# Performance work log

Hardware: AMD Instinct MI355X
Metric: run time of the kernel (lower is better)

The kernel has to match this reference:

```python
import jax, jax.numpy as jnp
import numpy as np

N_NODES = 100000
N_GRAPHS = 64

def gcn_conv(x, edge_index, W, b, num_nodes):
    # PyG GCNConv: x' = D^-1/2 (A + I) D^-1/2 (x W) + b
    h = x @ W  # [N, out]
    row, col = edge_index[0], edge_index[1]
    loops = jnp.arange(num_nodes, dtype=row.dtype)
    src = jnp.concatenate([row, loops])  # message source (x_j)
    dst = jnp.concatenate([col, loops])  # aggregation target
    deg = jax.ops.segment_sum(jnp.ones_like(src, dtype=h.dtype), dst,
                              num_segments=num_nodes)
    dinv = jnp.where(deg > 0, jax.lax.rsqrt(deg), 0.0)
    norm = dinv[src] * dinv[dst]  # [E+N]
    msgs = h[src] * norm[:, None]  # gather-transform
    out = jax.ops.segment_sum(msgs, dst, num_segments=num_nodes)  # scatter
    return out + b

def global_mean_pool(x, batch, num_graphs):
    sums = jax.ops.segment_sum(x, batch, num_segments=num_graphs)
    cnts = jax.ops.segment_sum(jnp.ones((x.shape[0],), x.dtype), batch,
                               num_segments=num_graphs)
    return sums / jnp.maximum(cnts, 1.0)[:, None]

def setup_inputs() -> dict:
    key = jax.random.key(0)
    ks = jax.random.split(key, 12)
    d_in, d_hid, d_mid, d_out = 128, 128, 20, 10
    n_edges = 1600000
    x = jax.random.normal(ks[0], (N_NODES, d_in), dtype=jnp.float32)
    edge_index = jax.random.randint(ks[1], (2, n_edges), 0, N_NODES, dtype=jnp.int64)
    batch = jnp.sort(jax.random.randint(ks[2], (N_NODES,), 0, N_GRAPHS, dtype=jnp.int64))
    def glorot(k, fan_in, fan_out):
        s = (6.0 / (fan_in + fan_out)) ** 0.5
        return jax.random.uniform(k, (fan_in, fan_out), jnp.float32, -s, s)
    return {
        "x": x, "edge_index": edge_index, "batch": batch,
        "W1": glorot(ks[3], d_in, d_hid), "b1": jnp.zeros((d_hid,), jnp.float32),
        "W2": glorot(ks[4], d_hid, d_hid), "b2": jnp.zeros((d_hid,), jnp.float32),
        "fc1_W": glorot(ks[5], d_hid, d_mid), "fc1_b": jnp.zeros((d_mid,), jnp.float32),
        "fc2_W": glorot(ks[6], d_mid, d_out), "fc2_b": jnp.zeros((d_out,), jnp.float32),
    }

def reference(x, edge_index, batch, W1, b1, W2, b2, fc1_W, fc1_b, fc2_W, fc2_b):
    # eval mode: dropout is identity
    h = gcn_conv(x, edge_index, W1, b1, N_NODES)
    h = jax.nn.elu(h)
    h = gcn_conv(h, edge_index, W2, b2, N_NODES)
    g = global_mean_pool(h, batch, N_GRAPHS)  # [G, hidden]
    g = jax.nn.relu(g @ fc1_W + fc1_b)
    g = g @ fc2_W + fc2_b
    return jax.nn.log_softmax(g, axis=1)
```

## Files before the change

### kernel.cpp

```cpp
#include <hip/hip_runtime.h>
#include <math.h>

#define DH 128
#define BCAP 16384

typedef __bf16 bf8_t __attribute__((ext_vector_type(8)));
typedef short short8 __attribute__((ext_vector_type(8)));
typedef float f4_t __attribute__((ext_vector_type(4)));
typedef float f2_t __attribute__((ext_vector_type(2)));

__device__ inline unsigned short f2b(float f) {
    unsigned int u = __builtin_bit_cast(unsigned int, f);
    u = u + 0x7fffu + ((u >> 16) & 1u);
    return (unsigned short)(u >> 16);
}
__device__ inline float b2f(unsigned short h) {
    return __builtin_bit_cast(float, (unsigned int)h << 16);
}

__global__ __launch_bounds__(256) void k_bucket(const int* __restrict__ row,
                                                const int* __restrict__ col,
                                                int E, int nbuck, int chunk,
                                                unsigned int* __restrict__ pairs,
                                                int* __restrict__ bcur) {
    __shared__ int lcnt[256];
    __shared__ int lbase[256];
    __shared__ unsigned int srec[2048];
    int t = threadIdx.x;
    int e0 = blockIdx.x * chunk;
    int e1 = min(e0 + chunk, E);
    lcnt[t] = 0;
    __syncthreads();
    for (int i = e0 + t; i < e1; i += 256) {
        int d = col[i];
        int b = d >> 9;
        int slot = atomicAdd(&lcnt[b], 1);
        srec[i - e0] = ((unsigned int)b << 22) | ((unsigned int)(d & 511) << 13)
                     | (unsigned int)slot;
    }
    __syncthreads();
    if (t < nbuck) {
        int c = lcnt[t];
        lbase[t] = (c > 0) ? atomicAdd(&bcur[t * 16], c) : 0;
    }
    __syncthreads();
    for (int i = e0 + t; i < e1; i += 256) {
        unsigned int r = srec[i - e0];
        int b = r >> 22;
        unsigned int dl = (r >> 13) & 511u;
        int slot = (int)(r & 8191u);
        int g = lbase[b] + slot;
        if (g < BCAP)
            pairs[(size_t)b * BCAP + g] = ((unsigned int)row[i] << 9) | dl;
    }
}

__global__ __launch_bounds__(512) void k_build(const unsigned int* __restrict__ pairs,
                                               const int* __restrict__ bcur,
                                               int nbuck, int N,
                                               int* __restrict__ off,
                                               int* __restrict__ dpd,
                                               float* __restrict__ dinv,
                                               int* __restrict__ csr) {
    __shared__ int cnt2[512];
    __shared__ int scn[512];
    __shared__ int curi[512];
    int b = blockIdx.x, t = threadIdx.x;
    int cnt = min(bcur[b * 16], BCAP);
    int base = b * BCAP;
    int node0 = b << 9;
    int nodes = min(512, N - node0);
    cnt2[t] = (t < nodes) ? 1 : 0;
    __syncthreads();
    const unsigned int* pp = pairs + (size_t)b * BCAP;
    for (int i = t; i < cnt; i += 512)
        atomicAdd(&cnt2[pp[i] & 511u], 1);
    __syncthreads();
    int c = cnt2[t];
    int pdv = (c + 15) & ~15;
    scn[t] = pdv;
    __syncthreads();
    for (int d = 1; d < 512; d <<= 1) {
        int v = (t >= d) ? scn[t - d] : 0;
        __syncthreads();
        scn[t] += v;
        __syncthreads();
    }
    int exc = min(scn[t] - pdv, BCAP);
    int avail = BCAP - exc;
    int pdc = min(pdv, avail);
    curi[t] = exc + 1;
    if (t < nodes) {
        off[node0 + t] = base + exc;
        dpd[node0 + t] = pdc;
        dinv[node0 + t] = rsqrtf((float)c);
        if (pdc > 0) csr[base + exc] = node0 + t;
        for (int k = c; k < pdc; k++) csr[base + exc + k] = N;
    }
    __syncthreads();
    for (int i = t; i < cnt; i += 512) {
        unsigned int p = pp[i];
        int d = (int)(p & 511u);
        int slot = atomicAdd(&curi[d], 1);
        if (slot < BCAP) csr[base + slot] = (int)(p >> 9);
    }
}

__global__ void k_prepW(const float* __restrict__ W1, const float* __restrict__ W2,
                        unsigned short* __restrict__ Wt1, unsigned short* __restrict__ Wt2,
                        unsigned int* __restrict__ t8zrow) {
    int t = blockIdx.x * blockDim.x + threadIdx.x;
    if (blockIdx.x == 0 && threadIdx.x < 32) t8zrow[threadIdx.x] = 0u;
    int v = t & 16383;
    int k = v >> 7, n = v & 127;
    if (t < 16384) {
        Wt1[n * DH + k] = f2b(W1[k * DH + n]);
    } else {
        int p = ((k & 15) << 3) | (k >> 4);
        Wt2[n * DH + p] = f2b(W2[k * DH + n]);
    }
}

__global__ __launch_bounds__(256) void k_gemm_mfma(const void* __restrict__ Xin, int x_is_bf16,
                                                   const unsigned short* __restrict__ Wt,
                                                   const float* __restrict__ dinv,
                                                   unsigned char* __restrict__ Y, int nrows) {
    __shared__ unsigned short Xs[64 * 136];
    __shared__ unsigned short Ws[128 * 136];
    int t = threadIdx.x;
    int row0 = blockIdx.x * 64;

    for (int v = t; v < 128 * 32; v += 256) {
        int n = v >> 5, kq = v & 31;
        ushort4 w = ((const ushort4*)Wt)[v];
        *(ushort4*)&Ws[n * 136 + kq * 4] = w;
    }
    if (x_is_bf16) {
        const unsigned short* X = (const unsigned short*)Xin;
        for (int v = t; v < 64 * 32; v += 256) {
            int r = v >> 5, cq = v & 31;
            int gr = row0 + r;
            ushort4 h;
            if (gr < nrows) h = ((const ushort4*)X)[(size_t)gr * 32 + cq];
            else { h.x = 0; h.y = 0; h.z = 0; h.w = 0; }
            *(ushort4*)&Xs[r * 136 + cq * 4] = h;
        }
    } else {
        const float* X = (const float*)Xin;
        for (int v = t; v < 64 * 32; v += 256) {
            int r = v >> 5, cq = v & 31;
            int gr = row0 + r;
            ushort4 h;
            if (gr < nrows) {
                float4 xv = ((const float4*)X)[(size_t)gr * 32 + cq];
                h.x = f2b(xv.x); h.y = f2b(xv.y); h.z = f2b(xv.z); h.w = f2b(xv.w);
            } else { h.x = 0; h.y = 0; h.z = 0; h.w = 0; }
            *(ushort4*)&Xs[r * 136 + cq * 4] = h;
        }
    }
    __syncthreads();

    int w = t >> 6;
    int lane = t & 63;
    int quad = lane >> 4;
    int l16 = lane & 15;
    int rw = w * 16;

    f4_t acc[8];
#pragma unroll
    for (int j = 0; j < 8; j++) acc[j] = (f4_t){0.f, 0.f, 0.f, 0.f};

#pragma unroll
    for (int kk = 0; kk < 4; kk++) {
        int k0 = kk * 32;
        bf8_t a = __builtin_bit_cast(bf8_t,
            *(const short8*)&Xs[(rw + l16) * 136 + k0 + quad * 8]);
#pragma unroll
        for (int j = 0; j < 8; j++) {
            bf8_t b = __builtin_bit_cast(bf8_t,
                *(const short8*)&Ws[(j * 16 + l16) * 136 + k0 + quad * 8]);
            acc[j] = __builtin_amdgcn_mfma_f32_16x16x32_bf16(a, b, acc[j], 0, 0, 0);
        }
    }

#pragma unroll
    for (int reg = 0; reg < 4; reg++) {
        int r = row0 + rw + quad * 4 + reg;
        if (r < nrows) {
            float dv = dinv[r];
            float v0 = acc[0][reg] * dv, v1 = acc[1][reg] * dv;
            float v2 = acc[2][reg] * dv, v3 = acc[3][reg] * dv;
            float v4 = acc[4][reg] * dv, v5 = acc[5][reg] * dv;
            float v6 = acc[6][reg] * dv, v7 = acc[7][reg] * dv;
            int d0 = __builtin_amdgcn_cvt_pk_fp8_f32(v0, v1, 0, false);
            d0 = __builtin_amdgcn_cvt_pk_fp8_f32(v2, v3, d0, true);
            int d1 = __builtin_amdgcn_cvt_pk_fp8_f32(v4, v5, 0, false);
            d1 = __builtin_amdgcn_cvt_pk_fp8_f32(v6, v7, d1, true);
            *(uint2*)&Y[(size_t)r * DH + l16 * 8] = make_uint2((unsigned)d0, (unsigned)d1);
        }
    }
}

#define AGG_ROUND(IDX)                                                     \
    {                                                                      \
        int ea = be + i;                                                   \
        unsigned v0 = ((unsigned)IDX(ea)     << 7) | l5b;                  \
        unsigned v1 = ((unsigned)IDX(ea + 1) << 7) | l5b;                  \
        unsigned v2 = ((unsigned)IDX(ea + 2) << 7) | l5b;                  \
        unsigned v3 = ((unsigned)IDX(ea + 3) << 7) | l5b;                  \
        unsigned v4 = ((unsigned)IDX(ea + 4) << 7) | l5b;                  \
        unsigned v5 = ((unsigned)IDX(ea + 5) << 7) | l5b;                  \
        unsigned v6 = ((unsigned)IDX(ea + 6) << 7) | l5b;                  \
        unsigned v7 = ((unsigned)IDX(ea + 7) << 7) | l5b;                  \
        unsigned int u0 = *(const unsigned int*)(Tb + v0);                 \
        unsigned int u1 = *(const unsigned int*)(Tb + v1);                 \
        unsigned int u2 = *(const unsigned int*)(Tb + v2);                 \
        unsigned int u3 = *(const unsigned int*)(Tb + v3);                 \
        unsigned int u4 = *(const unsigned int*)(Tb + v4);                 \
        unsigned int u5 = *(const unsigned int*)(Tb + v5);                 \
        unsigned int u6 = *(const unsigned int*)(Tb + v6);                 \
        unsigned int u7 = *(const unsigned int*)(Tb + v7);                 \
        accA01 += __builtin_amdgcn_cvt_pk_f32_fp8(u0, false);              \
        accA23 += __builtin_amdgcn_cvt_pk_f32_fp8(u0, true);               \
        accB01 += __builtin_amdgcn_cvt_pk_f32_fp8(u1, false);              \
        accB23 += __builtin_amdgcn_cvt_pk_f32_fp8(u1, true);               \
        accA01 += __builtin_amdgcn_cvt_pk_f32_fp8(u2, false);              \
        accA23 += __builtin_amdgcn_cvt_pk_f32_fp8(u2, true);               \
        accB01 += __builtin_amdgcn_cvt_pk_f32_fp8(u3, false);              \
        accB23 += __builtin_amdgcn_cvt_pk_f32_fp8(u3, true);               \
        accA01 += __builtin_amdgcn_cvt_pk_f32_fp8(u4, false);              \
        accA23 += __builtin_amdgcn_cvt_pk_f32_fp8(u4, true);               \
        accB01 += __builtin_amdgcn_cvt_pk_f32_fp8(u5, false);              \
        accB23 += __builtin_amdgcn_cvt_pk_f32_fp8(u5, true);               \
        accA01 += __builtin_amdgcn_cvt_pk_f32_fp8(u6, false);              \
        accA23 += __builtin_amdgcn_cvt_pk_f32_fp8(u6, true);               \
        accB01 += __builtin_amdgcn_cvt_pk_f32_fp8(u7, false);              \
        accB23 += __builtin_amdgcn_cvt_pk_f32_fp8(u7, true);               \
    }

__global__ __launch_bounds__(256) void k_agg(const unsigned char* __restrict__ T,
                                             unsigned short* __restrict__ Out,
                                             const float* __restrict__ dinv,
                                             const int* __restrict__ off,
                                             const int* __restrict__ dpd,
                                             const int* __restrict__ csr,
                                             const float* __restrict__ bias,
                                             int elu, int N) {
    __shared__ int ofs[16];
    __shared__ int pds[16];
    __shared__ float dv16[16];
    __shared__ int sidx[768];
    int t = threadIdx.x;
    int d0 = blockIdx.x * 16;
    if (t < 16) {
        int n = min(d0 + t, N - 1);
        ofs[t] = off[n];
        pds[t] = dpd[n];
        dv16[t] = dinv[n];
    }
    __syncthreads();
    int s0 = ofs[0];
    int span = ofs[15] + pds[15] - s0;
    int scnt = min(span, 768);
    for (int k = t; k < scnt; k += 256) sidx[k] = csr[s0 + k];
    __syncthreads();

    int w = t >> 6;
    int lane = t & 63;
    int half = lane >> 5;
    int l5 = lane & 31;
    unsigned l5b = (unsigned)(l5 << 2);
    const char* Tb = (const char*)T;

    int c0 = ((l5 & 1) << 6) | (l5 >> 1);
    float bb0 = bias[c0], bb1 = bias[c0 + 16], bb2 = bias[c0 + 32], bb3 = bias[c0 + 48];

    for (int ni = 0; ni < 4; ni++) {
        int nl = 4 * w + ni;
        int nd = d0 + nl;
        if (nd >= N) break;
        int eL = ofs[nl] - s0;
        int pd = pds[nl];
        int K = pd >> 1;
        int be = eL + half * K;

        f2_t accA01 = (f2_t){0.f, 0.f}, accA23 = (f2_t){0.f, 0.f};
        f2_t accB01 = (f2_t){0.f, 0.f}, accB23 = (f2_t){0.f, 0.f};

        if (eL + pd <= scnt) {
#define IDX_L(e) sidx[e]
            for (int i = 0; i < K; i += 8) AGG_ROUND(IDX_L)
#undef IDX_L
        } else {
            const int* gp = csr + s0;
#define IDX_G(e) gp[e]
            for (int i = 0; i < K; i += 8) AGG_ROUND(IDX_G)
#undef IDX_G
        }

        float a0 = accA01[0] + accB01[0];
        float a1 = accA01[1] + accB01[1];
        float a2 = accA23[0] + accB23[0];
        float a3 = accA23[1] + accB23[1];
        a0 += __shfl_xor(a0, 32);
        a1 += __shfl_xor(a1, 32);
        a2 += __shfl_xor(a2, 32);
        a3 += __shfl_xor(a3, 32);

        if (!half) {
            float dv = dv16[nl];
            float o0 = a0 * dv + bb0;
            float o1 = a1 * dv + bb1;
            float o2 = a2 * dv + bb2;
            float o3 = a3 * dv + bb3;
            if (elu) {
                o0 = o0 > 0.f ? o0 : __expf(o0) - 1.f;
                o1 = o1 > 0.f ? o1 : __expf(o1) - 1.f;
                o2 = o2 > 0.f ? o2 : __expf(o2) - 1.f;
                o3 = o3 > 0.f ? o3 : __expf(o3) - 1.f;
            }
            unsigned int p0 = (unsigned int)f2b(o0) | ((unsigned int)f2b(o1) << 16);
            unsigned int p1 = (unsigned int)f2b(o2) | ((unsigned int)f2b(o3) << 16);
            *(uint2*)&Out[(size_t)nd * DH + (l5 << 2)] = make_uint2(p0, p1);
        }
    }
}

__global__ __launch_bounds__(256) void k_pool(const unsigned int* __restrict__ H32,
                                              const int* __restrict__ batch,
                                              float* __restrict__ Gsum,
                                              int* __restrict__ cnts, int N) {
    int g = blockIdx.x;
    int p = blockIdx.y;
    int t = threadIdx.x;
    int lane = t & 63;
    int rg = t >> 6;
    int lo = 0, hi = N;
    while (lo < hi) { int m = (lo + hi) >> 1; if (batch[m] < g) lo = m + 1; else hi = m; }
    int s = lo;
    hi = N;
    while (lo < hi) { int m = (lo + hi) >> 1; if (batch[m] < g + 1) lo = m + 1; else hi = m; }
    int e = lo;
    int len = e - s;
    int parts = (int)gridDim.y;
    int chunk = (len + parts - 1) / parts;
    int i0 = s + p * chunk;
    int i1 = min(i0 + chunk, e);
    float a0 = 0.f, a1 = 0.f;
    for (int i = i0 + rg; i < i1; i += 4) {
        unsigned int v = H32[(size_t)i * 64 + lane];
        a0 += b2f((unsigned short)(v & 0xffffu));
        a1 += b2f((unsigned short)(v >> 16));
    }
    __shared__ float ps[4][DH];
    ps[rg][lane * 2] = a0;
    ps[rg][lane * 2 + 1] = a1;
    __syncthreads();
    if (t < DH) {
        float v = ps[0][t] + ps[1][t] + ps[2][t] + ps[3][t];
        atomicAdd(&Gsum[g * DH + t], v);
    }
    if (p == 0 && t == 0) cnts[g] = len;
}

__global__ __launch_bounds__(64) void k_head(const float* __restrict__ Gsum,
                                             const int* __restrict__ cnts,
                                             const float* __restrict__ W1,
                                             const float* __restrict__ b1,
                                             const float* __restrict__ W2,
                                             const float* __restrict__ b2,
                                             float* __restrict__ out) {
    int g = blockIdx.x;
    int t = threadIdx.x;
    __shared__ float gv[DH];
    __shared__ float mid[20];
    __shared__ float o[10];
    float inv = 1.f / fmaxf((float)cnts[g], 1.f);
    for (int i = t; i < DH; i += 64) {
        int c = ((i & 7) << 4) | (i >> 3);
        gv[c] = Gsum[g * DH + i] * inv;
    }
    __syncthreads();
    if (t < 20) {
        float a = b1[t];
        for (int k = 0; k < DH; k++) a += gv[k] * W1[k * 20 + t];
        mid[t] = fmaxf(a, 0.f);
    }
    __syncthreads();
    if (t < 10) {
        float a = b2[t];
        for (int k = 0; k < 20; k++) a += mid[k] * W2[k * 10 + t];
        o[t] = a;
    }
    __syncthreads();
    if (t == 0) {
        float m = -1e30f;
        for (int j = 0; j < 10; j++) m = fmaxf(m, o[j]);
        float ssum = 0.f;
        for (int j = 0; j < 10; j++) ssum += expf(o[j] - m);
        float l = logf(ssum);
        for (int j = 0; j < 10; j++) out[g * 10 + j] = o[j] - m - l;
    }
}

extern "C" void kernel_launch(void* const* d_in, const int* in_sizes, int n_in,
                              void* d_out, int out_size, void* d_ws, size_t ws_size,
                              hipStream_t stream) {
    const float* x    = (const float*)d_in[0];
    const int*   ei   = (const int*)d_in[1];
    const int*   batch= (const int*)d_in[2];
    const float* W1   = (const float*)d_in[3];
    const float* b1   = (const float*)d_in[4];
    const float* W2   = (const float*)d_in[5];
    const float* b2   = (const float*)d_in[6];
    const float* fc1W = (const float*)d_in[7];
    const float* fc1b = (const float*)d_in[8];
    const float* fc2W = (const float*)d_in[9];
    const float* fc2b = (const float*)d_in[10];
    float* out = (float*)d_out;

    int N = in_sizes[0] / DH;
    int E = in_sizes[1] / 2;
    int G = out_size / 10;
    int nbuck = (N + 511) >> 9;

    char* p = (char*)d_ws;
    auto alloc = [&](size_t bytes) {
        char* r = p;
        p += (bytes + 255) & ~(size_t)255;
        return r;
    };
    size_t pairs_bytes = (size_t)nbuck * BCAP * 4;
    size_t t8_bytes = (size_t)(N + 1) * DH;
    char* region = alloc(pairs_bytes > t8_bytes ? pairs_bytes : t8_bytes);
    unsigned int*   pairs = (unsigned int*)region;
    unsigned char*  t8    = (unsigned char*)region;
    unsigned short* a1 = (unsigned short*)alloc((size_t)N * DH * 2);
    int*   csr  = (int*)alloc((size_t)nbuck * BCAP * 4);
    int*   off  = (int*)alloc((size_t)N * 4);
    int*   dpd  = (int*)alloc((size_t)N * 4);
    float* dinv = (float*)alloc((size_t)N * 4);
    unsigned short* Wt1 = (unsigned short*)alloc(DH * DH * 2);
    unsigned short* Wt2 = (unsigned short*)alloc(DH * DH * 2);
    float* Gsum = (float*)alloc((size_t)G * DH * 4);
    int*   bcur = (int*)alloc(256 * 16 * 4);
    int*   cnts = (int*)alloc((size_t)G * 4);

    const int* row = ei;
    const int* col = ei + E;

    (void)hipMemsetAsync(Gsum, 0, (size_t)G * DH * 4 + 256 * 16 * 4, stream);

    const int chunk = 2048;
    int ablocks = (E + chunk - 1) / chunk;
    k_bucket<<<ablocks, 256, 0, stream>>>(row, col, E, nbuck, chunk, pairs, bcur);
    k_build<<<nbuck, 512, 0, stream>>>(pairs, bcur, nbuck, N, off, dpd, dinv, csr);
    k_prepW<<<128, 256, 0, stream>>>(W1, W2, Wt1, Wt2,
                                     (unsigned int*)(t8 + (size_t)N * DH));

    int gblocks = (N + 63) / 64;
    int mblocks = (N + 15) / 16;
    k_gemm_mfma<<<gblocks, 256, 0, stream>>>(x, 0, Wt1, dinv, t8, N);
    k_agg<<<mblocks, 256, 0, stream>>>(t8, a1, dinv, off, dpd, csr, b1, 1, N);
    k_gemm_mfma<<<gblocks, 256, 0, stream>>>(a1, 1, Wt2, dinv, t8, N);
    k_agg<<<mblocks, 256, 0, stream>>>(t8, a1, dinv, off, dpd, csr, b2, 0, N);

    dim3 pg(G, 32);
    k_pool<<<pg, 256, 0, stream>>>((const unsigned int*)a1, batch, Gsum, cnts, N);
    k_head<<<G, 64, 0, stream>>>(Gsum, cnts, fc1W, fc1b, fc2W, fc2b, out);
}
```

Measured before the change: 290.2 us.

## Sort bucketed edges in LDS before scatter and fold weight prep into bucket kernel

The bucketing kernel now does a block-wide prefix scan over the per-bucket counts and stages each chunk's (value, destination) records in shared memory in bucket-sorted order. The final global write then comes from a contiguous sorted sequence, so writes to the same bucket sit next to each other and coalesce better. The weight transpose and bf16 conversion kernel is merged into the bucket launch as 128 extra blocks, which saves one launch. The pairs and t8 buffers no longer share memory, so the workspace grows, and the scan and extra LDS traffic add per-block cost and use more shared memory.

```diff
diff --git a/kernel.cpp b/kernel.cpp
--- a/kernel.cpp
+++ b/kernel.cpp
@@ -20,13 +20,36 @@
 
 __global__ __launch_bounds__(256) void k_bucket(const int* __restrict__ row,
                                                 const int* __restrict__ col,
-                                                int E, int nbuck, int chunk,
+                                                int E, int nbuck, int chunk, int ablocks,
                                                 unsigned int* __restrict__ pairs,
-                                                int* __restrict__ bcur) {
+                                                int* __restrict__ bcur,
+                                                const float* __restrict__ W1,
+                                                const float* __restrict__ W2,
+                                                unsigned short* __restrict__ Wt1,
+                                                unsigned short* __restrict__ Wt2,
+                                                unsigned int* __restrict__ t8zrow) {
+    int t = threadIdx.x;
+    if ((int)blockIdx.x >= ablocks) {
+        int bid2 = (int)blockIdx.x - ablocks;
+        int g = bid2 * 256 + t;
+        if (bid2 == 0 && t < 32) t8zrow[t] = 0u;
+        int v = g & 16383;
+        int k = v >> 7, n = v & 127;
+        if (g < 16384) {
+            Wt1[n * DH + k] = f2b(W1[k * DH + n]);
+        } else {
+            int p = ((k & 15) << 3) | (k >> 4);
+            Wt2[n * DH + p] = f2b(W2[k * DH + n]);
+        }
+        return;
+    }
     __shared__ int lcnt[256];
     __shared__ int lbase[256];
+    __shared__ int scn[256];
+    __shared__ int lofs[256];
     __shared__ unsigned int srec[2048];
-    int t = threadIdx.x;
+    __shared__ unsigned int srt_val[2048];
+    __shared__ unsigned int srt_dst[2048];
     int e0 = blockIdx.x * chunk;
     int e1 = min(e0 + chunk, E);
     lcnt[t] = 0;
@@ -39,19 +62,35 @@
                      | (unsigned int)slot;
     }
     __syncthreads();
-    if (t < nbuck) {
-        int c = lcnt[t];
+    {
+        int c = (t < nbuck) ? lcnt[t] : 0;
         lbase[t] = (c > 0) ? atomicAdd(&bcur[t * 16], c) : 0;
-    }
+        scn[t] = c;
+    }
+    __syncthreads();
+    for (int d = 1; d < 256; d <<= 1) {
+        int v = (t >= d) ? scn[t - d] : 0;
+        __syncthreads();
+        scn[t] += v;
+        __syncthreads();
+    }
+    lofs[t] = scn[t] - ((t < nbuck) ? lcnt[t] : 0);
     __syncthreads();
     for (int i = e0 + t; i < e1; i += 256) {
         unsigned int r = srec[i - e0];
         int b = r >> 22;
         unsigned int dl = (r >> 13) & 511u;
         int slot = (int)(r & 8191u);
+        int p = lofs[b] + slot;
         int g = lbase[b] + slot;
-        if (g < BCAP)
-            pairs[(size_t)b * BCAP + g] = ((unsigned int)row[i] << 9) | dl;
+        srt_val[p] = ((unsigned int)row[i] << 9) | dl;
+        srt_dst[p] = (g < BCAP) ? (unsigned int)(b * BCAP + g) : 0xFFFFFFFFu;
+    }
+    __syncthreads();
+    int cnt = e1 - e0;
+    for (int i = t; i < cnt; i += 256) {
+        unsigned int d = srt_dst[i];
+        if (d != 0xFFFFFFFFu) pairs[d] = srt_val[i];
     }
 }
 
@@ -103,21 +142,6 @@
         int d = (int)(p & 511u);
         int slot = atomicAdd(&curi[d], 1);
         if (slot < BCAP) csr[base + slot] = (int)(p >> 9);
-    }
-}
-
-__global__ void k_prepW(const float* __restrict__ W1, const float* __restrict__ W2,
-                        unsigned short* __restrict__ Wt1, unsigned short* __restrict__ Wt2,
-                        unsigned int* __restrict__ t8zrow) {
-    int t = blockIdx.x * blockDim.x + threadIdx.x;
-    if (blockIdx.x == 0 && threadIdx.x < 32) t8zrow[threadIdx.x] = 0u;
-    int v = t & 16383;
-    int k = v >> 7, n = v & 127;
-    if (t < 16384) {
-        Wt1[n * DH + k] = f2b(W1[k * DH + n]);
-    } else {
-        int p = ((k & 15) << 3) | (k >> 4);
-        Wt2[n * DH + p] = f2b(W2[k * DH + n]);
     }
 }
 
@@ -430,11 +454,8 @@
         p += (bytes + 255) & ~(size_t)255;
         return r;
     };
-    size_t pairs_bytes = (size_t)nbuck * BCAP * 4;
-    size_t t8_bytes = (size_t)(N + 1) * DH;
-    char* region = alloc(pairs_bytes > t8_bytes ? pairs_bytes : t8_bytes);
-    unsigned int*   pairs = (unsigned int*)region;
-    unsigned char*  t8    = (unsigned char*)region;
+    unsigned int*   pairs = (unsigned int*)alloc((size_t)nbuck * BCAP * 4);
+    unsigned char*  t8    = (unsigned char*)alloc((size_t)(N + 1) * DH);
     unsigned short* a1 = (unsigned short*)alloc((size_t)N * DH * 2);
     int*   csr  = (int*)alloc((size_t)nbuck * BCAP * 4);
     int*   off  = (int*)alloc((size_t)N * 4);
@@ -453,10 +474,10 @@
 
     const int chunk = 2048;
     int ablocks = (E + chunk - 1) / chunk;
-    k_bucket<<<ablocks, 256, 0, stream>>>(row, col, E, nbuck, chunk, pairs, bcur);
+    k_bucket<<<ablocks + 128, 256, 0, stream>>>(row, col, E, nbuck, chunk, ablocks,
+                                                pairs, bcur, W1, W2, Wt1, Wt2,
+                                                (unsigned int*)(t8 + (size_t)N * DH));
     k_build<<<nbuck, 512, 0, stream>>>(pairs, bcur, nbuck, N, off, dpd, dinv, csr);
-    k_prepW<<<128, 256, 0, stream>>>(W1, W2, Wt1, Wt2,
-                                     (unsigned int*)(t8 + (size_t)N * DH));
 
     int gblocks = (N + 63) / 64;
     int mblocks = (N + 15) / 16;
```

Result: no change. 284.9 us (-1.8%).
